# Kernel tuning notes

Measured on AMD Instinct MI355X. Metric: run time of the kernel, lower is better.

The kernel has to match this reference:

```python
import math
import jax, jax.numpy as jnp
import numpy as np

X_DIM = 512
Y_DIM = 512
DS = 4
WH, WW = Y_DIM // DS, X_DIM // DS
RADIUS = 6          # search_radius
PATCH = 21          # patch_size
SIGMA = 1.0         # preprocess_sigma
DELTA = 0.2
MASK_TH = 0.05
RAIN_TH = 0.1


def _blur(x, sigma=SIGMA):
    # replicate-pad + depthwise 2D gaussian conv (matches _gaussian_blur2d)
    r = max(1, int(math.ceil(3.0 * sigma)))
    c = jnp.arange(-r, r + 1, dtype=x.dtype)
    k1 = jnp.exp(-(c * c) / (2.0 * sigma * sigma))
    k1 = k1 / jnp.sum(k1)
    k2 = jnp.outer(k1, k1)
    C = x.shape[1]
    kern = jnp.broadcast_to(k2[None, None], (C, 1, 2 * r + 1, 2 * r + 1))
    xp = jnp.pad(x, ((0, 0), (0, 0), (r, r), (r, r)), mode='edge')
    return jax.lax.conv_general_dilated(xp, kern, (1, 1), 'VALID',
                                        dimension_numbers=('NCHW', 'OIHW', 'NCHW'),
                                        feature_group_count=C)


def _resize(x, oh, ow):
    # torch bilinear, align_corners=False, no antialias
    ih, iw = x.shape[-2], x.shape[-1]
    def coords(o, i):
        s = (jnp.arange(o, dtype=jnp.float32) + 0.5) * (i / o) - 0.5
        s = jnp.maximum(s, 0.0)
        i0 = jnp.minimum(jnp.floor(s).astype(jnp.int32), i - 1)
        i1 = jnp.minimum(i0 + 1, i - 1)
        return i0, i1, s - i0.astype(jnp.float32)
    y0, y1, wy = coords(oh, ih)
    x0, x1, wx = coords(ow, iw)
    r0 = x[..., y0, :]
    r1 = x[..., y1, :]
    v00 = r0[..., x0]; v01 = r0[..., x1]
    v10 = r1[..., x0]; v11 = r1[..., x1]
    wy = wy[:, None]; wx = wx[None, :]
    return v00 * (1 - wy) * (1 - wx) + v01 * (1 - wy) * wx + v10 * wy * (1 - wx) + v11 * wy * wx


def _avg_pool(x, k):
    # avg_pool2d, stride 1, padding k//2, count_include_pad=True
    p = k // 2
    nd = x.ndim
    win = (1,) * (nd - 2) + (k, k)
    pads = ((0, 0),) * (nd - 2) + ((p, p), (p, p))
    s = jax.lax.reduce_window(x, 0.0, jax.lax.add, win, (1,) * nd, pads)
    return s / float(k * k)


def _prepare(f):
    w = jnp.log1p(jnp.maximum(f, 0.0))
    w = _resize(w, WH, WW)
    return _blur(w)


def _grid_sample_border(field, grid):
    # bilinear grid_sample, padding_mode='border', align_corners=True
    B, C, H, W = field.shape
    ix = jnp.clip((grid[..., 0] + 1.0) * 0.5 * (W - 1), 0.0, W - 1)
    iy = jnp.clip((grid[..., 1] + 1.0) * 0.5 * (H - 1), 0.0, H - 1)
    x0 = jnp.floor(ix).astype(jnp.int32); y0 = jnp.floor(iy).astype(jnp.int32)
    x1 = jnp.minimum(x0 + 1, W - 1); y1 = jnp.minimum(y0 + 1, H - 1)
    wx = (ix - x0)[..., None]; wy = (iy - y0)[..., None]
    b = jnp.arange(B)[:, None, None]
    v00 = field[b, :, y0, x0]; v01 = field[b, :, y0, x1]
    v10 = field[b, :, y1, x0]; v11 = field[b, :, y1, x1]  # each [B,H,W,C]
    out = v00 * (1 - wy) * (1 - wx) + v01 * (1 - wy) * wx + v10 * wy * (1 - wx) + v11 * wy * wx
    return jnp.transpose(out, (0, 3, 1, 2))


def setup_inputs() -> dict:
    key = jax.random.key(0)
    k1, k2, k3 = jax.random.split(key, 3)
    pred = jax.random.normal(k1, (16, 1, 512, 512), dtype=jnp.float32)
    target = jax.random.uniform(k2, (16, 1, 512, 512), dtype=jnp.float32)
    ref = jax.random.uniform(k3, (16, 1, 512, 512), dtype=jnp.float32)
    return {"pred": pred, "target": target, "ref": ref}


def reference(pred, target, ref):
    prev_w = _prepare(ref)      # [B,1,WH,WW]
    curr_w = _prepare(target)
    rain = (_resize(target, WH, WW) >= RAIN_TH).astype(jnp.float32)
    n = 2 * RADIUS + 1
    offs = jnp.arange(-RADIUS, RADIUS + 1)
    dys = jnp.repeat(offs, n)   # dy outer loop
    dxs = jnp.tile(offs, n)     # dx inner loop
    rows = jnp.arange(WH); cols = jnp.arange(WW)

    def shift_cost(dy, dx):
        # replicate-border shift of curr_w by (dy,dx), then local SSD (21x21 avg)
        sh = curr_w[:, :, jnp.clip(rows + dy, 0, WH - 1), :]
        sh = sh[:, :, :, jnp.clip(cols + dx, 0, WW - 1)]
        return _avg_pool((prev_w - sh) ** 2, PATCH)

    costs = jax.vmap(shift_cost)(dys, dxs)        # [S,B,1,WH,WW]
    best = jnp.argmin(costs, axis=0)[:, 0]        # [B,WH,WW] (first-min, matches torch)
    fx = dxs.astype(jnp.float32)[best][:, None] * rain   # [B,1,WH,WW]
    fy = dys.astype(jnp.float32)[best][:, None] * rain
    fx = _blur(fx) * rain
    fy = _blur(fy) * rain
    fx = _resize(fx, Y_DIM, X_DIM) * (X_DIM / WW)
    fy = _resize(fy, Y_DIM, X_DIM) * (Y_DIM / WH)

    yy, xx = jnp.meshgrid(jnp.linspace(-1.0, 1.0, Y_DIM),
                          jnp.linspace(-1.0, 1.0, X_DIM), indexing='ij')
    gx = xx[None] - fx[:, 0] * (2.0 / (X_DIM - 1))
    gy = yy[None] - fy[:, 0] * (2.0 / (Y_DIM - 1))
    teacher = jnp.maximum(_grid_sample_border(ref, jnp.stack([gx, gy], axis=-1)), 0.0)

    d = pred - teacher
    ad = jnp.abs(d)
    loss = jnp.where(ad < DELTA, 0.5 * d * d, DELTA * (ad - 0.5 * DELTA))  # huber
    mask = ((teacher > MASK_TH) | (target > MASK_TH)).astype(loss.dtype)
    return jnp.mean(loss * mask)
```

## Files before the change

kernel.cpp:

```cpp
#include <hip/hip_runtime.h>
#include <math.h>

#define BATCH 16
#define HR 512
#define LR 128
#define N_LR (BATCH*LR*LR)
#define N_HR (BATCH*HR*HR)
#define NSH 13
#define NSHIFT 169
#define TH 8
#define NW 8
#define NSLOT 16

template<bool B> struct BoolC { static constexpr bool value = B; };

__device__ __forceinline__ int clampi(int v, int lo, int hi){ return v<lo?lo:(v>hi?hi:v); }

__device__ __forceinline__ float gk(int t){
  const float e1 = 0.60653065971263342f;
  const float e2 = 0.13533528323661270f;
  const float e3 = 0.011108996538242306f;
  const float norm = 1.0f/(1.0f + 2.0f*(e1+e2+e3));
  int a = t < 0 ? -t : t;
  float v = (a==0) ? 1.0f : (a==1 ? e1 : (a==2 ? e2 : e3));
  return v*norm;
}

__global__ void k_downsample(const float* __restrict__ ref, const float* __restrict__ tar,
                             float* __restrict__ wref, float* __restrict__ wtar,
                             float* __restrict__ rain){
  int i = blockIdx.x*blockDim.x + threadIdx.x;
  if (i >= N_LR) return;
  int x = i & (LR-1); int y = (i >> 7) & (LR-1); int b = i >> 14;
  int base = b*HR*HR + (4*y+1)*HR + 4*x;
  float4 r1 = *(const float4*)(ref + base);
  float4 r2 = *(const float4*)(ref + base + HR);
  float4 t1 = *(const float4*)(tar + base);
  float4 t2 = *(const float4*)(tar + base + HR);
  float r00=r1.y, r01=r1.z, r10=r2.y, r11=r2.z;
  float t00=t1.y, t01=t1.z, t10=t2.y, t11=t2.z;
  wref[i] = 0.25f*(log1pf(fmaxf(r00,0.f))+log1pf(fmaxf(r01,0.f))
                 +log1pf(fmaxf(r10,0.f))+log1pf(fmaxf(r11,0.f)));
  wtar[i] = 0.25f*(log1pf(fmaxf(t00,0.f))+log1pf(fmaxf(t01,0.f))
                 +log1pf(fmaxf(t10,0.f))+log1pf(fmaxf(t11,0.f)));
  rain[i] = (0.25f*(t00+t01+t10+t11) >= 0.1f) ? 1.0f : 0.0f;
}

__global__ void k_blur2(const float* __restrict__ in0, const float* __restrict__ in1,
                        float* __restrict__ out0, float* __restrict__ out1){
  const int z = blockIdx.z;
  const float* in  = z ? in1 : in0;
  float* out       = z ? out1 : out0;
  const int r0 = blockIdx.x * 16;
  const int bb = blockIdx.y;
  const int tid = threadIdx.x;
  const float* I = in + (bb<<14);
  __shared__ float raw[22][LR];
  __shared__ float hb[22][LR];
  for (int idx = tid; idx < 22*LR; idx += 256){
    int lr = idx >> 7, c = idx & (LR-1);
    int gr = clampi(r0 - 3 + lr, 0, LR-1);
    raw[lr][c] = I[(gr<<7) + c];
  }
  __syncthreads();
  for (int idx = tid; idx < 22*LR; idx += 256){
    int lr = idx >> 7, c = idx & (LR-1);
    float s = 0.f;
    #pragma unroll
    for (int t=-3;t<=3;++t) s += gk(t)*raw[lr][clampi(c+t,0,LR-1)];
    hb[lr][c] = s;
  }
  __syncthreads();
  for (int idx = tid; idx < 16*LR; idx += 256){
    int lr = idx >> 7, c = idx & (LR-1);
    int i = r0 + lr;
    float s = 0.f;
    #pragma unroll
    for (int t=-3;t<=3;++t) s += gk(t)*hb[clampi(i+t,0,LR-1) - (r0-3)][c];
    out[(bb<<14) + (i<<7) + c] = s;
  }
}

__global__ void k_blur2f(const unsigned long long* __restrict__ best0,
                         const unsigned long long* __restrict__ best1,
                         const float* __restrict__ rain,
                         float* __restrict__ outx, float* __restrict__ outy){
  const int z = blockIdx.z;
  float* out = z ? outy : outx;
  const int r0 = blockIdx.x * 16;
  const int bb = blockIdx.y;
  const int tid = threadIdx.x;
  __shared__ float raw[22][LR];
  __shared__ float hb[22][LR];
  for (int idx = tid; idx < 22*LR; idx += 256){
    int lr = idx >> 7, c = idx & (LR-1);
    int gr = clampi(r0 - 3 + lr, 0, LR-1);
    int gi = (bb<<14) + (gr<<7) + c;
    unsigned long long k = best0[gi];
    unsigned long long k1 = best1[gi]; if (k1 < k) k = k1;
    int s = (int)(k & 0xffffffffULL);
    int f = z ? (s / NSH - 6) : (s % NSH - 6);
    raw[lr][c] = (float)f * rain[gi];
  }
  __syncthreads();
  for (int idx = tid; idx < 22*LR; idx += 256){
    int lr = idx >> 7, c = idx & (LR-1);
    float s = 0.f;
    #pragma unroll
    for (int t=-3;t<=3;++t) s += gk(t)*raw[lr][clampi(c+t,0,LR-1)];
    hb[lr][c] = s;
  }
  __syncthreads();
  for (int idx = tid; idx < 16*LR; idx += 256){
    int lr = idx >> 7, c = idx & (LR-1);
    int i = r0 + lr;
    float s = 0.f;
    #pragma unroll
    for (int t=-3;t<=3;++t) s += gk(t)*hb[clampi(i+t,0,LR-1) - (r0-3)][c];
    int gi = (bb<<14) + (i<<7) + c;
    out[gi] = s * rain[gi];
  }
}

template<int CTRL, int RM>
__device__ __forceinline__ float dpp_mov0(float x){
  return __int_as_float(__builtin_amdgcn_update_dpp(0, __float_as_int(x), CTRL, RM, 0xF, true));
}
__device__ __forceinline__ float prefix64(float x){
  x += dpp_mov0<0x111,0xF>(x);
  x += dpp_mov0<0x112,0xF>(x);
  x += dpp_mov0<0x114,0xF>(x);
  x += dpp_mov0<0x118,0xF>(x);
  x += dpp_mov0<0x142,0xA>(x);
  x += dpp_mov0<0x143,0xC>(x);
  return x;
}
__device__ __forceinline__ float bperm(int addr4, float v){
  return __int_as_float(__builtin_amdgcn_ds_bpermute(addr4, __float_as_int(v)));
}

struct TapCtx { int ia0, ib0, ia1, ib1; bool la0hi, lb0ok, lb1hi, selA, selB; };

__device__ __forceinline__ void horiz_update(const TapCtx& tc, float v0, float v1, int s,
                                             unsigned long long& k0ref, unsigned long long& k1ref){
  float pf0 = prefix64(v0);
  float pf1 = prefix64(v1);
  float T0 = __int_as_float(__builtin_amdgcn_readlane(__float_as_int(pf0), 63));
  float va = tc.selA ? pf0 : pf1;
  float vb = tc.selB ? pf0 : pf1;
  float a0 = bperm(tc.ia0, va) + (tc.la0hi ? T0 : 0.f);
  float b0 = tc.lb0ok ? bperm(tc.ib0, pf0) : 0.f;
  float a1 = bperm(tc.ia1, pf1) + T0;
  float b1 = bperm(tc.ib1, vb) + (tc.lb1hi ? T0 : 0.f);
  float c0 = fmaxf((a0 - b0) * (1.0f/441.0f), 0.f);
  float c1 = fmaxf((a1 - b1) * (1.0f/441.0f), 0.f);
  unsigned long long k0 = ((unsigned long long)__float_as_uint(c0) << 32) | (unsigned)s;
  unsigned long long k1 = ((unsigned long long)__float_as_uint(c1) << 32) | (unsigned)s;
  if (k0 < k0ref) k0ref = k0;
  if (k1 < k1ref) k1ref = k1;
}

__global__ void __launch_bounds__(512, 2)
k_cost_flow(const float* __restrict__ prev, const float* __restrict__ curr,
            unsigned long long* __restrict__ best0,
            unsigned long long* __restrict__ best1){
  const int r0 = blockIdx.x * TH;
  const int bb = blockIdx.y;
  const int z  = blockIdx.z;
  const int tid = threadIdx.x;
  const int w = tid >> 6, lane = tid & 63;
  const float* P = prev + (bb<<14);
  const float* C = curr + (bb<<14);

  __shared__ float currT[40][LR];
  __shared__ unsigned long long mg[4][TH*LR];

  for (int idx = tid; idx < 40*LR; idx += 512){
    int lr = idx >> 7, c = idx & (LR-1);
    int gr = clampi(r0 - 16 + lr, 0, LR-1);
    currT[lr][c] = C[(gr<<7) + c];
  }

  float p0[28], p1[28];
  #pragma unroll
  for (int wr = 0; wr < 28; ++wr){
    int gr = r0 - 10 + wr;
    if (gr >= 0 && gr < LR){ p0[wr] = P[(gr<<7) + lane]; p1[wr] = P[(gr<<7) + lane + 64]; }
    else                   { p0[wr] = 0.f; p1[wr] = 0.f; }
  }
  __syncthreads();

  unsigned long long bk0[TH], bk1[TH];
  #pragma unroll
  for (int io = 0; io < TH; ++io){ bk0[io] = ~0ULL; bk1[io] = ~0ULL; }

  TapCtx tc;
  tc.ia0 = ((lane + 10) & 63) << 2;
  tc.ib0 = ((lane - 11) & 63) << 2;
  tc.ia1 = (min(lane + 10, 63)) << 2;
  tc.ib1 = ((lane + 53) & 63) << 2;
  tc.la0hi = (lane >= 54);
  tc.lb0ok = (lane >= 11);
  tc.lb1hi = (lane >= 11);
  tc.selA  = (lane >= 10);
  tc.selB  = (lane >= 53);

  const int slot = z*NW + w;
  const int t_lo = (NSHIFT * slot) / NSLOT;
  const int t_hi = (NSHIFT * (slot+1)) / NSLOT;

  auto walk = [&](auto CHK){
    constexpr bool chk = decltype(CHK)::value;
    int t = t_lo;
    while (t < t_hi){
      const int dxi  = t / NSH;
      const int dyi0 = t - dxi*NSH;
      const int ndy  = min(NSH - dyi0, t_hi - t);
      const int dx   = dxi - 6;
      const int c0   = clampi(lane + dx, 0, LR-1);
      const int c1   = clampi(lane + 64 + dx, 0, LR-1);
      float q0[28], q1[28];
      #pragma unroll
      for (int wr = 0; wr < 28; ++wr){
        q0[wr] = currT[wr + dyi0][c0];
        q1[wr] = currT[wr + dyi0][c1];
      }
      int s = dyi0*NSH + dxi;
      for (int rep = 0; rep < ndy; ++rep){
        float v0 = 0.f, v1 = 0.f;
        #pragma unroll
        for (int wr = 0; wr <= 20; ++wr){
          if (!chk || (r0 - 10 + wr >= 0 && r0 - 10 + wr < LR)){
            float d0 = p0[wr] - q0[wr];
            float d1 = p1[wr] - q1[wr];
            v0 = fmaf(d0, d0, v0);
            v1 = fmaf(d1, d1, v1);
          }
        }
        horiz_update(tc, v0, v1, s, bk0[0], bk1[0]);
        #pragma unroll
        for (int io = 1; io < TH; ++io){
          {
            const int wrA = io + 20;
            if (!chk || (r0 - 10 + wrA < LR)){
              float d0 = p0[wrA] - q0[wrA];
              float d1 = p1[wrA] - q1[wrA];
              v0 = fmaf(d0, d0, v0);
              v1 = fmaf(d1, d1, v1);
            }
            const int wrS = io - 1;
            if (!chk || (r0 - 10 + wrS >= 0)){
              float d0 = p0[wrS] - q0[wrS];
              float d1 = p1[wrS] - q1[wrS];
              v0 = fmaf(-d0, d0, v0);
              v1 = fmaf(-d1, d1, v1);
            }
          }
          horiz_update(tc, v0, v1, s, bk0[io], bk1[io]);
        }
        if (rep < ndy - 1){
          #pragma unroll
          for (int wr = 0; wr < 27; ++wr){ q0[wr] = q0[wr+1]; q1[wr] = q1[wr+1]; }
          q0[27] = currT[dyi0 + rep + 28][c0];
          q1[27] = currT[dyi0 + rep + 28][c1];
        }
        s += NSH;
      }
      t += ndy;
    }
  };
  if (r0 >= 16 && r0 <= 104) walk(BoolC<false>{});
  else                       walk(BoolC<true>{});

  __syncthreads();
  const int g = w & 3;
  if (w < 4){
    #pragma unroll
    for (int io = 0; io < TH; ++io){
      mg[g][io*LR + lane]      = bk0[io];
      mg[g][io*LR + lane + 64] = bk1[io];
    }
  }
  __syncthreads();
  if (w >= 4){
    #pragma unroll
    for (int io = 0; io < TH; ++io){
      unsigned long long m0 = mg[g][io*LR + lane];
      unsigned long long m1 = mg[g][io*LR + lane + 64];
      mg[g][io*LR + lane]      = (bk0[io] < m0) ? bk0[io] : m0;
      mg[g][io*LR + lane + 64] = (bk1[io] < m1) ? bk1[io] : m1;
    }
  }
  __syncthreads();
  unsigned long long* best = z ? best1 : best0;
  for (int p = tid; p < TH*LR; p += 512){
    unsigned long long k  = mg[0][p];
    unsigned long long k1 = mg[1][p]; if (k1 < k) k = k1;
    unsigned long long k2 = mg[2][p]; if (k2 < k) k = k2;
    unsigned long long k3 = mg[3][p]; if (k3 < k) k = k3;
    int io = p >> 7, jj = p & (LR-1);
    best[(bb<<14) + ((r0+io)<<7) + jj] = k;
  }
}

__global__ void __launch_bounds__(256)
k_loss(const float* __restrict__ pred, const float* __restrict__ tar,
       const float* __restrict__ ref, const float* __restrict__ fxb,
       const float* __restrict__ fyb, float* __restrict__ out){
  const int t0 = blockIdx.x*256 + threadIdx.x;
  float acc = 0.f;
  #pragma unroll
  for (int it = 0; it < 2; ++it){
    const int gq  = t0 + it*524288;
    const int b   = gq >> 16;
    const int rem = gq & 65535;
    const int y   = rem >> 7;
    const int m   = rem & 127;
    const int n = y >> 2, ky = y & 3;
    int y0; float wy;
    if (ky < 2){ y0 = max(n-1, 0); wy = (n >= 1) ? (ky == 0 ? 0.625f : 0.875f) : 0.f; }
    else       { y0 = n;           wy = (ky == 2) ? 0.125f : 0.375f; }
    const int y1 = min(y0+1, LR-1);
    const int lb = b << 14;
    const float* FxR0 = fxb + lb + (y0<<7);
    const float* FxR1 = fxb + lb + (y1<<7);
    const float* FyR0 = fyb + lb + (y0<<7);
    const float* FyR1 = fyb + lb + (y1<<7);
    const int cA = max(m-1, 0), cB = m, cC = min(m+1, LR-1);
    float xA0 = FxR0[cA], xB0 = FxR0[cB], xC0 = FxR0[cC];
    float xA1 = FxR1[cA], xB1 = FxR1[cB], xC1 = FxR1[cC];
    float yA0 = FyR0[cA], yB0 = FyR0[cB], yC0 = FyR0[cC];
    float yA1 = FyR1[cA], yB1 = FyR1[cB], yC1 = FyR1[cC];
    const bool mh = (m >= 1);
    const int hb = (b<<18) + (y<<9) + (m<<2);
    float4 pd = *(const float4*)(pred + hb);
    float4 td = *(const float4*)(tar + hb);
    const float* R = ref + (b<<18);
    const float wy1 = 1.f - wy;
    #pragma unroll
    for (int k = 0; k < 4; ++k){
      float wx;
      float lo0, hi0, lo1, hi1, flo0, fhi0, flo1, fhi1;
      if (k < 2){
        wx = mh ? (k == 0 ? 0.625f : 0.875f) : 0.f;
        lo0 = mh ? xA0 : xB0;  hi0 = mh ? xB0 : xC0;
        lo1 = mh ? xA1 : xB1;  hi1 = mh ? xB1 : xC1;
        flo0 = mh ? yA0 : yB0; fhi0 = mh ? yB0 : yC0;
        flo1 = mh ? yA1 : yB1; fhi1 = mh ? yB1 : yC1;
      } else {
        wx = (k == 2) ? 0.125f : 0.375f;
        lo0 = xB0;  hi0 = xC0;  lo1 = xB1;  hi1 = xC1;
        flo0 = yB0; fhi0 = yC0; flo1 = yB1; fhi1 = yC1;
      }
      const float w00 = wy1*(1.f-wx), w01 = wy1*wx, w10 = wy*(1.f-wx), w11 = wy*wx;
      const float fxv = 4.f*(w00*lo0 + w01*hi0 + w10*lo1 + w11*hi1);
      const float fyv = 4.f*(w00*flo0 + w01*fhi0 + w10*flo1 + w11*fhi1);
      const int x = (m<<2) + k;
      float ix = fminf(fmaxf((float)x - fxv, 0.f), (float)(HR-1));
      float iy = fminf(fmaxf((float)y - fyv, 0.f), (float)(HR-1));
      int gx0 = (int)ix; int gx1 = min(gx0+1, HR-1); float gwx = ix - (float)gx0;
      int gy0 = (int)iy; int gy1 = min(gy0+1, HR-1); float gwy = iy - (float)gy0;
      float v00 = R[(gy0<<9)+gx0], v01 = R[(gy0<<9)+gx1];
      float v10 = R[(gy1<<9)+gx0], v11 = R[(gy1<<9)+gx1];
      float tt = v00*(1.f-gwy)*(1.f-gwx) + v01*(1.f-gwy)*gwx
               + v10*gwy*(1.f-gwx)       + v11*gwy*gwx;
      float teacher = fmaxf(tt, 0.f);
      float pk = ((const float*)&pd)[k];
      float tk = ((const float*)&td)[k];
      float d  = pk - teacher;
      float ad = fabsf(d);
      float l  = ad < 0.2f ? 0.5f*d*d : 0.2f*(ad - 0.1f);
      float mm = (teacher > 0.05f || tk > 0.05f) ? 1.f : 0.f;
      acc += l*mm;
    }
  }
  acc *= (1.0f/(float)N_HR);
  #pragma unroll
  for (int o = 32; o > 0; o >>= 1) acc += __shfl_down(acc, o, 64);
  __shared__ float wsum[4];
  int lane = threadIdx.x & 63, wv = threadIdx.x >> 6;
  if (lane == 0) wsum[wv] = acc;
  __syncthreads();
  if (threadIdx.x == 0) atomicAdd(out, wsum[0]+wsum[1]+wsum[2]+wsum[3]);
}

extern "C" void kernel_launch(void* const* d_in, const int* in_sizes, int n_in,
                              void* d_out, int out_size, void* d_ws, size_t ws_size,
                              hipStream_t stream){
  const float* pred = (const float*)d_in[0];
  const float* tar  = (const float*)d_in[1];
  const float* ref  = (const float*)d_in[2];
  float* out = (float*)d_out;
  float* w = (float*)d_ws;
  float* prevW = w + 0*N_LR;
  float* currW = w + 1*N_LR;
  float* rain  = w + 2*N_LR;
  float* fxb   = w + 3*N_LR;
  float* fyb   = w + 4*N_LR;
  float* dsA   = w + 5*N_LR;
  float* dsB   = w + 6*N_LR;
  unsigned long long* best0 = (unsigned long long*)(w + 7*N_LR);
  unsigned long long* best1 = best0 + N_LR;

  hipMemsetAsync(d_out, 0, sizeof(float), stream);

  const int tb = 256, nb = (N_LR + tb - 1)/tb;
  k_downsample<<<nb, tb, 0, stream>>>(ref, tar, dsA, dsB, rain);
  k_blur2<<<dim3(8, BATCH, 2), tb, 0, stream>>>(dsA, dsB, prevW, currW);
  k_cost_flow<<<dim3(LR/TH, BATCH, 2), 512, 0, stream>>>(prevW, currW, best0, best1);
  k_blur2f<<<dim3(8, BATCH, 2), tb, 0, stream>>>(best0, best1, rain, fxb, fyb);
  k_loss<<<2048, tb, 0, stream>>>(pred, tar, ref, fxb, fyb, out);
}
```

Measured before the change: 199.8 us.

## Shrink per-thread register windows by streaming added rows from LDS

Reduces the per-thread prev and curr row windows from 28 to 21 registers each. The 7 extra rows needed by the sliding vertical sum are now read from a new shared-memory prevL buffer and directly from currT inside the inner loop. This lowers register pressure, which may help occupancy or avoid spills under the 512x2 launch bounds, at the cost of more LDS reads per shift. It also merges the ib1 bpermute index into ib0, which appear to be equal modulo 64, saving one register.

```diff
diff --git a/kernel.cpp b/kernel.cpp
--- a/kernel.cpp
+++ b/kernel.cpp
@@ -139,7 +139,7 @@
   return __int_as_float(__builtin_amdgcn_ds_bpermute(addr4, __float_as_int(v)));
 }
 
-struct TapCtx { int ia0, ib0, ia1, ib1; bool la0hi, lb0ok, lb1hi, selA, selB; };
+struct TapCtx { int ia0, ib0, ia1; bool la0hi, lb0ok, lb1hi, selA, selB; };
 
 __device__ __forceinline__ void horiz_update(const TapCtx& tc, float v0, float v1, int s,
                                              unsigned long long& k0ref, unsigned long long& k1ref){
@@ -151,7 +151,7 @@
   float a0 = bperm(tc.ia0, va) + (tc.la0hi ? T0 : 0.f);
   float b0 = tc.lb0ok ? bperm(tc.ib0, pf0) : 0.f;
   float a1 = bperm(tc.ia1, pf1) + T0;
-  float b1 = bperm(tc.ib1, vb) + (tc.lb1hi ? T0 : 0.f);
+  float b1 = bperm(tc.ib0, vb) + (tc.lb1hi ? T0 : 0.f);
   float c0 = fmaxf((a0 - b0) * (1.0f/441.0f), 0.f);
   float c1 = fmaxf((a1 - b1) * (1.0f/441.0f), 0.f);
   unsigned long long k0 = ((unsigned long long)__float_as_uint(c0) << 32) | (unsigned)s;
@@ -173,6 +173,7 @@
   const float* C = curr + (bb<<14);
 
   __shared__ float currT[40][LR];
+  __shared__ float prevL[7][LR];
   __shared__ unsigned long long mg[4][TH*LR];
 
   for (int idx = tid; idx < 40*LR; idx += 512){
@@ -180,13 +181,18 @@
     int gr = clampi(r0 - 16 + lr, 0, LR-1);
     currT[lr][c] = C[(gr<<7) + c];
   }
-
-  float p0[28], p1[28];
+  for (int idx = tid; idx < 7*LR; idx += 512){
+    int j = idx >> 7, c = idx & (LR-1);
+    int gr = r0 + 11 + j;
+    prevL[j][c] = (gr < LR) ? P[(gr<<7) + c] : 0.f;
+  }
+
+  float p0[21], p1[21];
   #pragma unroll
-  for (int wr = 0; wr < 28; ++wr){
-    int gr = r0 - 10 + wr;
-    if (gr >= 0 && gr < LR){ p0[wr] = P[(gr<<7) + lane]; p1[wr] = P[(gr<<7) + lane + 64]; }
-    else                   { p0[wr] = 0.f; p1[wr] = 0.f; }
+  for (int k = 0; k < 21; ++k){
+    int gr = r0 - 10 + k;
+    if (gr >= 0 && gr < LR){ p0[k] = P[(gr<<7) + lane]; p1[k] = P[(gr<<7) + lane + 64]; }
+    else                   { p0[k] = 0.f; p1[k] = 0.f; }
   }
   __syncthreads();
 
@@ -198,7 +204,6 @@
   tc.ia0 = ((lane + 10) & 63) << 2;
   tc.ib0 = ((lane - 11) & 63) << 2;
   tc.ia1 = (min(lane + 10, 63)) << 2;
-  tc.ib1 = ((lane + 53) & 63) << 2;
   tc.la0hi = (lane >= 54);
   tc.lb0ok = (lane >= 11);
   tc.lb1hi = (lane >= 11);
@@ -219,50 +224,52 @@
       const int dx   = dxi - 6;
       const int c0   = clampi(lane + dx, 0, LR-1);
       const int c1   = clampi(lane + 64 + dx, 0, LR-1);
-      float q0[28], q1[28];
+      float q0[21], q1[21];
       #pragma unroll
-      for (int wr = 0; wr < 28; ++wr){
-        q0[wr] = currT[wr + dyi0][c0];
-        q1[wr] = currT[wr + dyi0][c1];
+      for (int k = 0; k < 21; ++k){
+        q0[k] = currT[k + dyi0][c0];
+        q1[k] = currT[k + dyi0][c1];
       }
       int s = dyi0*NSH + dxi;
       for (int rep = 0; rep < ndy; ++rep){
+        const int dyi = dyi0 + rep;
         float v0 = 0.f, v1 = 0.f;
         #pragma unroll
-        for (int wr = 0; wr <= 20; ++wr){
-          if (!chk || (r0 - 10 + wr >= 0 && r0 - 10 + wr < LR)){
-            float d0 = p0[wr] - q0[wr];
-            float d1 = p1[wr] - q1[wr];
+        for (int k = 0; k <= 20; ++k){
+          if (!chk || (r0 - 10 + k >= 0 && r0 - 10 + k < LR)){
+            float d0 = p0[k] - q0[k];
+            float d1 = p1[k] - q1[k];
             v0 = fmaf(d0, d0, v0);
             v1 = fmaf(d1, d1, v1);
           }
         }
         horiz_update(tc, v0, v1, s, bk0[0], bk1[0]);
+        float sav0 = 0.f, sav1 = 0.f;
         #pragma unroll
         for (int io = 1; io < TH; ++io){
-          {
-            const int wrA = io + 20;
-            if (!chk || (r0 - 10 + wrA < LR)){
-              float d0 = p0[wrA] - q0[wrA];
-              float d1 = p1[wrA] - q1[wrA];
-              v0 = fmaf(d0, d0, v0);
-              v1 = fmaf(d1, d1, v1);
-            }
-            const int wrS = io - 1;
-            if (!chk || (r0 - 10 + wrS >= 0)){
-              float d0 = p0[wrS] - q0[wrS];
-              float d1 = p1[wrS] - q1[wrS];
-              v0 = fmaf(-d0, d0, v0);
-              v1 = fmaf(-d1, d1, v1);
-            }
+          float qa0 = currT[dyi + io + 20][c0];
+          float qa1 = currT[dyi + io + 20][c1];
+          if (io == 1){ sav0 = qa0; sav1 = qa1; }
+          if (!chk || (r0 + io + 10 < LR)){
+            float pa0 = prevL[io-1][lane];
+            float pa1 = prevL[io-1][lane + 64];
+            float d0 = pa0 - qa0;
+            float d1 = pa1 - qa1;
+            v0 = fmaf(d0, d0, v0);
+            v1 = fmaf(d1, d1, v1);
+          }
+          if (!chk || (r0 + io - 11 >= 0)){
+            float d0 = p0[io-1] - q0[io-1];
+            float d1 = p1[io-1] - q1[io-1];
+            v0 = fmaf(-d0, d0, v0);
+            v1 = fmaf(-d1, d1, v1);
           }
           horiz_update(tc, v0, v1, s, bk0[io], bk1[io]);
         }
         if (rep < ndy - 1){
           #pragma unroll
-          for (int wr = 0; wr < 27; ++wr){ q0[wr] = q0[wr+1]; q1[wr] = q1[wr+1]; }
-          q0[27] = currT[dyi0 + rep + 28][c0];
-          q1[27] = currT[dyi0 + rep + 28][c1];
+          for (int k = 0; k < 20; ++k){ q0[k] = q0[k+1]; q1[k] = q1[k+1]; }
+          q0[20] = sav0; q1[20] = sav1;
         }
         s += NSH;
       }
```

New measurement: 203.4 us. No clear change (+1.8%).
